# Kernel optimization log

Measured on AMD Instinct MI355X. Metric: run time of the kernel, lower is better.

## Reference

```python
import jax, jax.numpy as jnp
import numpy as np

B, S, D, V = 64, 128, 64, 50000

def _prelu(x, a):
    return jnp.where(x >= 0, x, a * x)

def setup_inputs() -> dict:
    key = jax.random.key(0)
    ks = jax.random.split(key, 24)
    stdv = 1.0 / np.sqrt(D)
    u = lambda k, shape: jax.random.uniform(k, shape, jnp.float32, -stdv, stdv)
    emb = u(ks[0], (V, D)).at[0].set(0.0)  # padding_idx=0
    inp = {
        'items': jax.random.randint(ks[1], (B, S), 0, V),
        'A': jax.random.randint(ks[2], (B, S, S), 0, 2),
        'edgeorder': jax.random.randint(ks[3], (B, S, S), 0, S),
        'last_nodes': jax.random.randint(ks[4], (B,), 0, S),
        'mask': jnp.ones((B, S), dtype=bool),
        'emb': emb,
        'W_self': u(ks[5], (D, D)), 'W_neigh': u(ks[6], (D, D)),
        'prelu1': jnp.full((D,), 0.25, jnp.float32),
        'Wq': u(ks[7], (D, D)), 'bq': jnp.zeros((D,), jnp.float32),
        'Wk': u(ks[8], (D, D)), 'Wv': u(ks[9], (D, D)), 'we': u(ks[10], (D,)),
        'prelu2': jnp.full((D,), 0.25, jnp.float32),
        'Wu': u(ks[11], (D, D)), 'bu': jnp.zeros((D,), jnp.float32),
        'Wvr': u(ks[12], (D, D)), 'wer': u(ks[13], (D,)),
        'prelu3': jnp.full((D,), 0.25, jnp.float32),
        'W_sr': u(ks[14], (2 * D, D)),
    }
    return inp

def reference(items, A, edgeorder, last_nodes, mask, emb, W_self, W_neigh, prelu1,
              Wq, bq, Wk, Wv, we, prelu2, Wu, bu, Wvr, wer, prelu3, W_sr):
    x = emb[items]  # [B,S,D]
    # ---- EOPA: masked neighbor broadcast + edgeorder gather + max-pool ----
    adjT = (jnp.swapaxes(A, 1, 2) == 1)  # [B,S(target),S(neighbor)]
    neigh = jnp.where((adjT & mask[:, None, :])[..., None], x[:, None, :, :], 0.0)  # [B,S,S,D]
    eo_t = jnp.swapaxes(edgeorder, 1, 2)  # [B,S,S]
    # gathered[b,i,j,:] = neigh[b, edgeorder[b,j,i], j, :]
    neigh = jnp.take_along_axis(neigh, eo_t[..., None], axis=1)
    neigh = neigh.max(axis=2)  # [B,S,D]
    h = _prelu(x @ W_self + neigh @ W_neigh, prelu1)
    # ---- SGAT: sigmoid-gated attention over adjacency ----
    q = h @ Wq + bq
    k = h @ Wk
    v = h @ Wv
    e = k[:, :, None, :] + q[:, None, :, :]             # e[b,i,j,d]
    e = jnp.where((A == 1)[..., None], e, 0.0)
    e = jax.nn.sigmoid(e) @ we                           # [B,S,S]
    a = jax.nn.softmax(e, axis=1)                        # softmax over source i
    h2 = _prelu(jnp.einsum('bij,bid->bjd', a, v), prelu2)
    # ---- AttnReadout ----
    xu = h2 @ Wu + bu                                    # [B,S,D]
    xlast = h2[jnp.arange(h2.shape[0]), last_nodes]      # [B,D]
    xv = xlast @ Wvr
    eatt = jax.nn.sigmoid(xu + xv[:, None, :]) @ wer     # [B,S]
    alpha = jax.nn.softmax(eatt, axis=1)
    out = _prelu((h2 * alpha[..., None]).sum(axis=1), prelu3)  # [B,D]
    # ---- session representation ----
    sr = jnp.concatenate([out, xlast], axis=-1) @ W_sr   # [B,D]
    return sr
```

## Files before the change

### kernel.cpp

```cpp
#include <hip/hip_runtime.h>

#define BB 64
#define SS 128
#define DD 64
#define SSQ (SS*SS)
#define BSD (BB*SS*DD)

__device__ __forceinline__ float fast_sigmoid(float x) {
  return __builtin_amdgcn_rcpf(1.0f + __expf(-x));
}

__global__ __launch_bounds__(256) void kA(
    const int* __restrict__ items, const int* __restrict__ Aadj,
    const int* __restrict__ eo, const float* __restrict__ emb,
    const float* __restrict__ Wself, const float* __restrict__ Wneigh,
    const float* __restrict__ prelu1,
    const float* __restrict__ Wq, const float* __restrict__ bq,
    const float* __restrict__ Wk, const float* __restrict__ Wv,
    float* __restrict__ q_ws, float* __restrict__ k_ws, float* __restrict__ v_ws)
{
  __shared__ alignas(16) float xs[SS*DD];
  __shared__ alignas(16) float Wb[2][DD*DD];
  __shared__ alignas(16) float nms[16*DD];
  __shared__ alignas(16) float hs[16*DD];
  __shared__ unsigned short condw[SS];
  const int b  = blockIdx.x >> 3;
  const int i0 = (blockIdx.x & 7) * 16;
  const int tid = threadIdx.x;
  const int wv = tid >> 6, lane = tid & 63;

  {
    const float4* emb4 = (const float4*)emb;
    float4* xs4 = (float4*)xs;
    for (int f = tid; f < SS*16; f += 256) {
      int j = f >> 4, qd = f & 15;
      xs4[f] = emb4[items[b*SS + j]*16 + qd];
    }
    const float4* W4 = (const float4*)Wself;
    float4* Wb4 = (float4*)Wb[0];
    for (int f = tid; f < 1024; f += 256) Wb4[f] = W4[f];
  }
  {
    int eov[8];
#pragma unroll
    for (int k = 0; k < 8; k++) {
      int p = tid + k*256;
      eov[k] = eo[b*SSQ + (p >> 4)*SS + i0 + (p & 15)];
    }
#pragma unroll
    for (int k = 0; k < 8; k++) {
      int p = tid + k*256;
      bool c = (Aadj[b*SSQ + (p >> 4)*SS + eov[k]] == 1);
      unsigned long long bm = __ballot(c);
      if ((lane & 15) == 0)
        condw[p >> 4] = (unsigned short)(bm >> lane);
    }
  }
  __syncthreads();

  {
    const float4* W4 = (const float4*)Wneigh;
    float4* Wb4 = (float4*)Wb[1];
    for (int f = tid; f < 1024; f += 256) Wb4[f] = W4[f];
  }
  {
    float m[4];
#pragma unroll
    for (int t = 0; t < 4; t++) m[t] = -__builtin_inff();
    for (int j = 0; j < SS; j++) {
      unsigned int cw = (unsigned int)condw[j] >> (wv*4);
      float xv = xs[j*DD + lane];
#pragma unroll
      for (int t = 0; t < 4; t++) {
        float val = ((cw >> t) & 1u) ? xv : 0.0f;
        m[t] = fmaxf(m[t], val);
      }
    }
#pragma unroll
    for (int t = 0; t < 4; t++) nms[(wv*4 + t)*DD + lane] = m[t];
  }
  float acc[4];
#pragma unroll
  for (int t = 0; t < 4; t++) acc[t] = 0.0f;
  for (int kk = 0; kk < DD; kk++) {
    float w = Wb[0][kk*DD + lane];
#pragma unroll
    for (int t = 0; t < 4; t++)
      acc[t] = fmaf(xs[(i0 + wv*4 + t)*DD + kk], w, acc[t]);
  }
  __syncthreads();

  {
    const float4* W4 = (const float4*)Wq;
    float4* Wb4 = (float4*)Wb[0];
    for (int f = tid; f < 1024; f += 256) Wb4[f] = W4[f];
  }
  for (int kk = 0; kk < DD; kk++) {
    float w = Wb[1][kk*DD + lane];
#pragma unroll
    for (int t = 0; t < 4; t++)
      acc[t] = fmaf(nms[(wv*4 + t)*DD + kk], w, acc[t]);
  }
  {
    float p1 = prelu1[lane];
#pragma unroll
    for (int t = 0; t < 4; t++) {
      float h = acc[t];
      hs[(wv*4 + t)*DD + lane] = (h >= 0.0f) ? h : p1*h;
    }
  }
  __syncthreads();

  const int r0g = b*SS + i0;
  {
    const float4* W4 = (const float4*)Wk;
    float4* Wb4 = (float4*)Wb[1];
    for (int f = tid; f < 1024; f += 256) Wb4[f] = W4[f];
  }
  {
    float bqv = bq[lane];
#pragma unroll
    for (int t = 0; t < 4; t++) acc[t] = bqv;
    for (int kk = 0; kk < DD; kk++) {
      float w = Wb[0][kk*DD + lane];
#pragma unroll
      for (int t = 0; t < 4; t++)
        acc[t] = fmaf(hs[(wv*4 + t)*DD + kk], w, acc[t]);
    }
#pragma unroll
    for (int t = 0; t < 4; t++) q_ws[(r0g + wv*4 + t)*DD + lane] = acc[t];
  }
  __syncthreads();

  {
    const float4* W4 = (const float4*)Wv;
    float4* Wb4 = (float4*)Wb[0];
    for (int f = tid; f < 1024; f += 256) Wb4[f] = W4[f];
  }
  {
#pragma unroll
    for (int t = 0; t < 4; t++) acc[t] = 0.0f;
    for (int kk = 0; kk < DD; kk++) {
      float w = Wb[1][kk*DD + lane];
#pragma unroll
      for (int t = 0; t < 4; t++)
        acc[t] = fmaf(hs[(wv*4 + t)*DD + kk], w, acc[t]);
    }
#pragma unroll
    for (int t = 0; t < 4; t++) k_ws[(r0g + wv*4 + t)*DD + lane] = acc[t];
  }
  __syncthreads();

  {
#pragma unroll
    for (int t = 0; t < 4; t++) acc[t] = 0.0f;
    for (int kk = 0; kk < DD; kk++) {
      float w = Wb[0][kk*DD + lane];
#pragma unroll
      for (int t = 0; t < 4; t++)
        acc[t] = fmaf(hs[(wv*4 + t)*DD + kk], w, acc[t]);
    }
#pragma unroll
    for (int t = 0; t < 4; t++) v_ws[(r0g + wv*4 + t)*DD + lane] = acc[t];
  }
}

__global__ __launch_bounds__(256) void kB(
    const int* __restrict__ Aadj,
    const float* __restrict__ q_ws, const float* __restrict__ k_ws,
    const float* __restrict__ v_ws,
    const float* __restrict__ we, const float* __restrict__ prelu2,
    const float* __restrict__ Wu, const float* __restrict__ bu,
    float* __restrict__ h2_ws, float* __restrict__ xu_ws)
{
  __shared__ alignas(16) float ks[SS*65];
  __shared__ alignas(16) float qs[16*65];
  __shared__ alignas(16) float es[16*129];
  __shared__ float wes[DD];
  const int b  = blockIdx.x >> 3;
  const int j0 = (blockIdx.x & 7) * 16;
  const int tid = threadIdx.x;
  const int wv = tid >> 6, lane = tid & 63;

  {
    const float4* k4 = (const float4*)k_ws;
    for (int f = tid; f < 2048; f += 256) {
      int i = f >> 4, d4 = f & 15;
      float4 v = k4[(b*SS + i)*16 + d4];
      float* dst = &ks[i*65 + d4*4];
      dst[0] = v.x; dst[1] = v.y; dst[2] = v.z; dst[3] = v.w;
    }
    const float4* q4 = (const float4*)q_ws;
    for (int f = tid; f < 256; f += 256) {
      int jl = f >> 4, d4 = f & 15;
      float4 v = q4[(b*SS + j0 + jl)*16 + d4];
      float* dst = &qs[jl*65 + d4*4];
      dst[0] = v.x; dst[1] = v.y; dst[2] = v.z; dst[3] = v.w;
    }
  }
  if (tid < DD) wes[tid] = we[tid];
  float hw = we[lane];
  for (int off = 32; off >= 1; off >>= 1) hw += __shfl_xor(hw, off);
  const float half_sum = 0.5f * hw;
  __syncthreads();

#pragma unroll
  for (int k = 0; k < 8; k++) {
    int p = tid + k*256;
    int jl = p & 15, i = p >> 4;
    float e2;
    if (Aadj[b*SSQ + i*SS + j0 + jl] == 1) {
      float s = 0.0f;
      for (int d2 = 0; d2 < DD; d2++) {
        float t = ks[i*65 + d2] + qs[jl*65 + d2];
        s = fmaf(wes[d2], fast_sigmoid(t), s);
      }
      e2 = s;
    } else {
      e2 = half_sum;
    }
    es[jl*129 + i] = e2;
  }
  __syncthreads();

  float* vs = ks;
  {
    const float4* v4 = (const float4*)v_ws;
    float4* vs4 = (float4*)vs;
    for (int f = tid; f < 2048; f += 256)
      vs4[f] = v4[b*SS*16 + f];
  }
#pragma unroll
  for (int t = 0; t < 4; t++) {
    int jl = wv*4 + t;
    float a0 = es[jl*129 + lane], a1 = es[jl*129 + 64 + lane];
    float mx = fmaxf(a0, a1);
    for (int off = 32; off >= 1; off >>= 1) mx = fmaxf(mx, __shfl_xor(mx, off));
    float p0 = __expf(a0 - mx), p1 = __expf(a1 - mx);
    float sm = p0 + p1;
    for (int off = 32; off >= 1; off >>= 1) sm += __shfl_xor(sm, off);
    float inv = 1.0f / sm;
    es[jl*129 + lane]      = p0 * inv;
    es[jl*129 + 64 + lane] = p1 * inv;
  }
  __syncthreads();

  float acc[4];
#pragma unroll
  for (int t = 0; t < 4; t++) acc[t] = 0.0f;
  for (int i = 0; i < SS; i++) {
    float vv = vs[i*DD + lane];
#pragma unroll
    for (int t = 0; t < 4; t++)
      acc[t] = fmaf(es[(wv*4 + t)*129 + i], vv, acc[t]);
  }
  float h2r[4];
  {
    float p2 = prelu2[lane];
#pragma unroll
    for (int t = 0; t < 4; t++) {
      float h2 = acc[t];
      h2r[t] = (h2 >= 0.0f) ? h2 : p2*h2;
      h2_ws[(b*SS + j0 + wv*4 + t)*DD + lane] = h2r[t];
    }
  }
  __syncthreads();

  float* hs2 = es;
  float* Wus = ks;
#pragma unroll
  for (int t = 0; t < 4; t++) hs2[(wv*4 + t)*DD + lane] = h2r[t];
  {
    const float4* W4 = (const float4*)Wu;
    float4* Wus4 = (float4*)Wus;
    for (int f = tid; f < 1024; f += 256) Wus4[f] = W4[f];
  }
  __syncthreads();
  {
    float buv = bu[lane];
    float acc2[4];
#pragma unroll
    for (int t = 0; t < 4; t++) acc2[t] = buv;
    for (int kk = 0; kk < DD; kk++) {
      float w = Wus[kk*DD + lane];
#pragma unroll
      for (int t = 0; t < 4; t++)
        acc2[t] = fmaf(hs2[(wv*4 + t)*DD + kk], w, acc2[t]);
    }
#pragma unroll
    for (int t = 0; t < 4; t++)
      xu_ws[(b*SS + j0 + wv*4 + t)*DD + lane] = acc2[t];
  }
}

__global__ __launch_bounds__(512) void k4_readout(
    const float* __restrict__ h2_ws, const float* __restrict__ xu_ws,
    const int* __restrict__ last_nodes,
    const float* __restrict__ Wvr, const float* __restrict__ wer,
    const float* __restrict__ prelu3, const float* __restrict__ Wsr,
    float* __restrict__ out)
{
  __shared__ float xlast[DD], xv[DD], eatt[SS], alpha[SS], outs[DD];
  __shared__ float pools[8*DD];
  const int b = blockIdx.x;
  const int tid = threadIdx.x;
  const int wv = tid >> 6, lane = tid & 63;

  const int ln = last_nodes[b];
  if (tid < DD) xlast[tid] = h2_ws[(b*SS + ln)*DD + tid];
  __syncthreads();
  if (tid < DD) {
    float s = 0.0f;
    for (int k2 = 0; k2 < DD; k2++)
      s = fmaf(xlast[k2], Wvr[k2*DD + tid], s);
    xv[tid] = s;
  }
  __syncthreads();
  {
    float werv = wer[lane];
    float xvl = xv[lane];
    for (int j = wv; j < SS; j += 8) {
      float xuv = xu_ws[(b*SS + j)*DD + lane];
      float term = fast_sigmoid(xuv + xvl) * werv;
      for (int off = 32; off >= 1; off >>= 1) term += __shfl_xor(term, off);
      if (lane == 0) eatt[j] = term;
    }
  }
  __syncthreads();
  if (wv == 0) {
    float a0 = eatt[lane], a1 = eatt[64 + lane];
    float mx = fmaxf(a0, a1);
    for (int off = 32; off >= 1; off >>= 1) mx = fmaxf(mx, __shfl_xor(mx, off));
    float p0 = __expf(a0 - mx), p1 = __expf(a1 - mx);
    float sm = p0 + p1;
    for (int off = 32; off >= 1; off >>= 1) sm += __shfl_xor(sm, off);
    float inv = 1.0f / sm;
    alpha[lane]      = p0 * inv;
    alpha[64 + lane] = p1 * inv;
  }
  __syncthreads();
  {
    float part = 0.0f;
    for (int j = wv; j < SS; j += 8)
      part = fmaf(alpha[j], h2_ws[(b*SS + j)*DD + lane], part);
    pools[wv*DD + lane] = part;
  }
  __syncthreads();
  if (wv == 0) {
    float s = 0.0f;
#pragma unroll
    for (int w = 0; w < 8; w++) s += pools[w*DD + lane];
    float p3 = prelu3[lane];
    outs[lane] = (s >= 0.0f) ? s : p3 * s;
  }
  __syncthreads();
  {
    float fs = 0.0f;
    for (int m2 = wv*16; m2 < wv*16 + 16; m2++) {
      float src = (m2 < DD) ? outs[m2] : xlast[m2 - DD];
      fs = fmaf(src, Wsr[m2*DD + lane], fs);
    }
    pools[wv*DD + lane] = fs;
  }
  __syncthreads();
  if (wv == 0) {
    float s = 0.0f;
#pragma unroll
    for (int w = 0; w < 8; w++) s += pools[w*DD + lane];
    out[b*DD + lane] = s;
  }
}

extern "C" void kernel_launch(void* const* d_in, const int* in_sizes, int n_in,
                              void* d_out, int out_size, void* d_ws, size_t ws_size,
                              hipStream_t stream)
{
  const int* items = (const int*)d_in[0];
  const int* Aadj  = (const int*)d_in[1];
  const int* eo    = (const int*)d_in[2];
  const int* lastn = (const int*)d_in[3];
  const float* emb    = (const float*)d_in[5];
  const float* Wself  = (const float*)d_in[6];
  const float* Wneigh = (const float*)d_in[7];
  const float* p1     = (const float*)d_in[8];
  const float* Wq     = (const float*)d_in[9];
  const float* bq     = (const float*)d_in[10];
  const float* Wk     = (const float*)d_in[11];
  const float* Wv     = (const float*)d_in[12];
  const float* we     = (const float*)d_in[13];
  const float* p2     = (const float*)d_in[14];
  const float* Wu     = (const float*)d_in[15];
  const float* bu     = (const float*)d_in[16];
  const float* Wvr    = (const float*)d_in[17];
  const float* wer    = (const float*)d_in[18];
  const float* p3     = (const float*)d_in[19];
  const float* Wsr    = (const float*)d_in[20];

  float* ws    = (float*)d_ws;
  float* q_ws  = ws;
  float* k_ws  = ws + (size_t)BSD;
  float* v_ws  = ws + (size_t)2*BSD;
  float* h2_ws = ws + (size_t)3*BSD;
  float* xu_ws = ws + (size_t)4*BSD;

  kA<<<BB*8, 256, 0, stream>>>(items, Aadj, eo, emb, Wself, Wneigh, p1,
                               Wq, bq, Wk, Wv, q_ws, k_ws, v_ws);
  kB<<<BB*8, 256, 0, stream>>>(Aadj, q_ws, k_ws, v_ws, we, p2, Wu, bu,
                               h2_ws, xu_ws);
  k4_readout<<<BB, 512, 0, stream>>>(h2_ws, xu_ws, lastn, Wvr, wer, p3, Wsr,
                                     (float*)d_out);
}
```

Baseline: 183.8 us.

## Halve rows per block, use readlane matvecs, drop LDS weight staging

Kernels kA and kB now handle 8 rows per block instead of 16, doubling the grid to 1024 blocks and cutting LDS use so more blocks fit per CU. Weight matrices are read directly from global/L2 rather than staged in shared memory. Per-row activations stay in registers and are broadcast with readlane, which removes several __syncthreads and LDS round trips. kB also makes the sigmoid loop branch-free, and the readout spreads the Wvr matvec across all waves. The cost is that each block reloads the full 128-row key/value set and the embeddings, and the weights are refetched from global memory instead of LDS.

```diff
diff --git a/kernel.cpp b/kernel.cpp
--- a/kernel.cpp
+++ b/kernel.cpp
@@ -9,8 +9,11 @@
 __device__ __forceinline__ float fast_sigmoid(float x) {
   return __builtin_amdgcn_rcpf(1.0f + __expf(-x));
 }
-
-__global__ __launch_bounds__(256) void kA(
+__device__ __forceinline__ float rl(float v, int l) {
+  return __int_as_float(__builtin_amdgcn_readlane(__float_as_int(v), l));
+}
+
+__global__ __launch_bounds__(256, 4) void kA(
     const int* __restrict__ items, const int* __restrict__ Aadj,
     const int* __restrict__ eo, const float* __restrict__ emb,
     const float* __restrict__ Wself, const float* __restrict__ Wneigh,
@@ -20,12 +23,9 @@
     float* __restrict__ q_ws, float* __restrict__ k_ws, float* __restrict__ v_ws)
 {
   __shared__ alignas(16) float xs[SS*DD];
-  __shared__ alignas(16) float Wb[2][DD*DD];
-  __shared__ alignas(16) float nms[16*DD];
-  __shared__ alignas(16) float hs[16*DD];
-  __shared__ unsigned short condw[SS];
-  const int b  = blockIdx.x >> 3;
-  const int i0 = (blockIdx.x & 7) * 16;
+  __shared__ unsigned char condw[SS];
+  const int b  = blockIdx.x >> 4;
+  const int i0 = (blockIdx.x & 15) * 8;
   const int tid = threadIdx.x;
   const int wv = tid >> 6, lane = tid & 63;
 
@@ -36,136 +36,102 @@
       int j = f >> 4, qd = f & 15;
       xs4[f] = emb4[items[b*SS + j]*16 + qd];
     }
-    const float4* W4 = (const float4*)Wself;
-    float4* Wb4 = (float4*)Wb[0];
-    for (int f = tid; f < 1024; f += 256) Wb4[f] = W4[f];
-  }
-  {
-    int eov[8];
-#pragma unroll
-    for (int k = 0; k < 8; k++) {
-      int p = tid + k*256;
-      eov[k] = eo[b*SSQ + (p >> 4)*SS + i0 + (p & 15)];
-    }
-#pragma unroll
-    for (int k = 0; k < 8; k++) {
-      int p = tid + k*256;
-      bool c = (Aadj[b*SSQ + (p >> 4)*SS + eov[k]] == 1);
+  }
+  {
+    int eov[4];
+#pragma unroll
+    for (int kq = 0; kq < 4; kq++) {
+      int p = tid + kq*256;
+      eov[kq] = eo[b*SSQ + (p >> 3)*SS + i0 + (p & 7)];
+    }
+#pragma unroll
+    for (int kq = 0; kq < 4; kq++) {
+      int p = tid + kq*256;
+      bool c = (Aadj[b*SSQ + (p >> 3)*SS + eov[kq]] == 1);
       unsigned long long bm = __ballot(c);
-      if ((lane & 15) == 0)
-        condw[p >> 4] = (unsigned short)(bm >> lane);
-    }
-  }
-  __syncthreads();
-
-  {
-    const float4* W4 = (const float4*)Wneigh;
-    float4* Wb4 = (float4*)Wb[1];
-    for (int f = tid; f < 1024; f += 256) Wb4[f] = W4[f];
-  }
-  {
-    float m[4];
-#pragma unroll
-    for (int t = 0; t < 4; t++) m[t] = -__builtin_inff();
-    for (int j = 0; j < SS; j++) {
-      unsigned int cw = (unsigned int)condw[j] >> (wv*4);
-      float xv = xs[j*DD + lane];
-#pragma unroll
-      for (int t = 0; t < 4; t++) {
-        float val = ((cw >> t) & 1u) ? xv : 0.0f;
-        m[t] = fmaxf(m[t], val);
-      }
-    }
-#pragma unroll
-    for (int t = 0; t < 4; t++) nms[(wv*4 + t)*DD + lane] = m[t];
-  }
-  float acc[4];
-#pragma unroll
-  for (int t = 0; t < 4; t++) acc[t] = 0.0f;
+      if ((lane & 7) == 0)
+        condw[p >> 3] = (unsigned char)(bm >> lane);
+    }
+  }
+  __syncthreads();
+
+  float m[2];
+#pragma unroll
+  for (int t = 0; t < 2; t++) m[t] = -__builtin_inff();
+  for (int j = 0; j < SS; j++) {
+    unsigned int cw = (unsigned int)condw[j] >> (wv*2);
+    float xv = xs[j*DD + lane];
+#pragma unroll
+    for (int t = 0; t < 2; t++) {
+      float val = ((cw >> t) & 1u) ? xv : 0.0f;
+      m[t] = fmaxf(m[t], val);
+    }
+  }
+  float xr[2];
+#pragma unroll
+  for (int t = 0; t < 2; t++) xr[t] = xs[(i0 + wv*2 + t)*DD + lane];
+
+  float acc[2] = {0.0f, 0.0f};
+#pragma unroll 8
   for (int kk = 0; kk < DD; kk++) {
-    float w = Wb[0][kk*DD + lane];
-#pragma unroll
-    for (int t = 0; t < 4; t++)
-      acc[t] = fmaf(xs[(i0 + wv*4 + t)*DD + kk], w, acc[t]);
-  }
-  __syncthreads();
-
-  {
-    const float4* W4 = (const float4*)Wq;
-    float4* Wb4 = (float4*)Wb[0];
-    for (int f = tid; f < 1024; f += 256) Wb4[f] = W4[f];
-  }
+    float w = Wself[kk*DD + lane];
+#pragma unroll
+    for (int t = 0; t < 2; t++) acc[t] = fmaf(rl(xr[t], kk), w, acc[t]);
+  }
+#pragma unroll 8
   for (int kk = 0; kk < DD; kk++) {
-    float w = Wb[1][kk*DD + lane];
-#pragma unroll
-    for (int t = 0; t < 4; t++)
-      acc[t] = fmaf(nms[(wv*4 + t)*DD + kk], w, acc[t]);
-  }
+    float w = Wneigh[kk*DD + lane];
+#pragma unroll
+    for (int t = 0; t < 2; t++) acc[t] = fmaf(rl(m[t], kk), w, acc[t]);
+  }
+  float hr[2];
   {
     float p1 = prelu1[lane];
 #pragma unroll
-    for (int t = 0; t < 4; t++) {
+    for (int t = 0; t < 2; t++) {
       float h = acc[t];
-      hs[(wv*4 + t)*DD + lane] = (h >= 0.0f) ? h : p1*h;
-    }
-  }
-  __syncthreads();
-
-  const int r0g = b*SS + i0;
-  {
-    const float4* W4 = (const float4*)Wk;
-    float4* Wb4 = (float4*)Wb[1];
-    for (int f = tid; f < 1024; f += 256) Wb4[f] = W4[f];
-  }
+      hr[t] = (h >= 0.0f) ? h : p1*h;
+    }
+  }
+
+  const int r0g = b*SS + i0 + wv*2;
   {
     float bqv = bq[lane];
-#pragma unroll
-    for (int t = 0; t < 4; t++) acc[t] = bqv;
+    float a2[2] = {bqv, bqv};
+#pragma unroll 8
     for (int kk = 0; kk < DD; kk++) {
-      float w = Wb[0][kk*DD + lane];
-#pragma unroll
-      for (int t = 0; t < 4; t++)
-        acc[t] = fmaf(hs[(wv*4 + t)*DD + kk], w, acc[t]);
-    }
-#pragma unroll
-    for (int t = 0; t < 4; t++) q_ws[(r0g + wv*4 + t)*DD + lane] = acc[t];
-  }
-  __syncthreads();
-
-  {
-    const float4* W4 = (const float4*)Wv;
-    float4* Wb4 = (float4*)Wb[0];
-    for (int f = tid; f < 1024; f += 256) Wb4[f] = W4[f];
-  }
-  {
-#pragma unroll
-    for (int t = 0; t < 4; t++) acc[t] = 0.0f;
+      float w = Wq[kk*DD + lane];
+#pragma unroll
+      for (int t = 0; t < 2; t++) a2[t] = fmaf(rl(hr[t], kk), w, a2[t]);
+    }
+#pragma unroll
+    for (int t = 0; t < 2; t++) q_ws[(r0g + t)*DD + lane] = a2[t];
+  }
+  {
+    float a2[2] = {0.0f, 0.0f};
+#pragma unroll 8
     for (int kk = 0; kk < DD; kk++) {
-      float w = Wb[1][kk*DD + lane];
-#pragma unroll
-      for (int t = 0; t < 4; t++)
-        acc[t] = fmaf(hs[(wv*4 + t)*DD + kk], w, acc[t]);
-    }
-#pragma unroll
-    for (int t = 0; t < 4; t++) k_ws[(r0g + wv*4 + t)*DD + lane] = acc[t];
-  }
-  __syncthreads();
-
-  {
-#pragma unroll
-    for (int t = 0; t < 4; t++) acc[t] = 0.0f;
+      float w = Wk[kk*DD + lane];
+#pragma unroll
+      for (int t = 0; t < 2; t++) a2[t] = fmaf(rl(hr[t], kk), w, a2[t]);
+    }
+#pragma unroll
+    for (int t = 0; t < 2; t++) k_ws[(r0g + t)*DD + lane] = a2[t];
+  }
+  {
+    float a2[2] = {0.0f, 0.0f};
+#pragma unroll 8
     for (int kk = 0; kk < DD; kk++) {
-      float w = Wb[0][kk*DD + lane];
-#pragma unroll
-      for (int t = 0; t < 4; t++)
-        acc[t] = fmaf(hs[(wv*4 + t)*DD + kk], w, acc[t]);
-    }
-#pragma unroll
-    for (int t = 0; t < 4; t++) v_ws[(r0g + wv*4 + t)*DD + lane] = acc[t];
-  }
-}
-
-__global__ __launch_bounds__(256) void kB(
+      float w = Wv[kk*DD + lane];
+#pragma unroll
+      for (int t = 0; t < 2; t++) a2[t] = fmaf(rl(hr[t], kk), w, a2[t]);
+    }
+#pragma unroll
+    for (int t = 0; t < 2; t++) v_ws[(r0g + t)*DD + lane] = a2[t];
+  }
+}
+
+__global__ __launch_bounds__(256, 4) void kB(
     const int* __restrict__ Aadj,
     const float* __restrict__ q_ws, const float* __restrict__ k_ws,
     const float* __restrict__ v_ws,
@@ -174,11 +140,11 @@
     float* __restrict__ h2_ws, float* __restrict__ xu_ws)
 {
   __shared__ alignas(16) float ks[SS*65];
-  __shared__ alignas(16) float qs[16*65];
-  __shared__ alignas(16) float es[16*129];
+  __shared__ alignas(16) float qs[8*65];
+  __shared__ alignas(16) float es[8*129];
   __shared__ float wes[DD];
-  const int b  = blockIdx.x >> 3;
-  const int j0 = (blockIdx.x & 7) * 16;
+  const int b  = blockIdx.x >> 4;
+  const int j0 = (blockIdx.x & 15) * 8;
   const int tid = threadIdx.x;
   const int wv = tid >> 6, lane = tid & 63;
 
@@ -191,35 +157,30 @@
       dst[0] = v.x; dst[1] = v.y; dst[2] = v.z; dst[3] = v.w;
     }
     const float4* q4 = (const float4*)q_ws;
-    for (int f = tid; f < 256; f += 256) {
-      int jl = f >> 4, d4 = f & 15;
+    if (tid < 128) {
+      int jl = tid >> 4, d4 = tid & 15;
       float4 v = q4[(b*SS + j0 + jl)*16 + d4];
       float* dst = &qs[jl*65 + d4*4];
       dst[0] = v.x; dst[1] = v.y; dst[2] = v.z; dst[3] = v.w;
     }
-  }
-  if (tid < DD) wes[tid] = we[tid];
+    if (tid < DD) wes[tid] = we[tid];
+  }
   float hw = we[lane];
   for (int off = 32; off >= 1; off >>= 1) hw += __shfl_xor(hw, off);
   const float half_sum = 0.5f * hw;
   __syncthreads();
 
 #pragma unroll
-  for (int k = 0; k < 8; k++) {
-    int p = tid + k*256;
-    int jl = p & 15, i = p >> 4;
-    float e2;
-    if (Aadj[b*SSQ + i*SS + j0 + jl] == 1) {
-      float s = 0.0f;
-      for (int d2 = 0; d2 < DD; d2++) {
-        float t = ks[i*65 + d2] + qs[jl*65 + d2];
-        s = fmaf(wes[d2], fast_sigmoid(t), s);
-      }
-      e2 = s;
-    } else {
-      e2 = half_sum;
-    }
-    es[jl*129 + i] = e2;
+  for (int kq = 0; kq < 4; kq++) {
+    int p = tid + kq*256;
+    int jl = p & 7, i = p >> 3;
+    bool isE = (Aadj[b*SSQ + i*SS + j0 + jl] == 1);
+    float s = 0.0f;
+    for (int d2 = 0; d2 < DD; d2++) {
+      float t = ks[i*65 + d2] + qs[jl*65 + d2];
+      s = fmaf(wes[d2], fast_sigmoid(t), s);
+    }
+    es[jl*129 + i] = isE ? s : half_sum;
   }
   __syncthreads();
 
@@ -230,9 +191,10 @@
     for (int f = tid; f < 2048; f += 256)
       vs4[f] = v4[b*SS*16 + f];
   }
-#pragma unroll
-  for (int t = 0; t < 4; t++) {
-    int jl = wv*4 + t;
+  float a0n[2], a1n[2];
+#pragma unroll
+  for (int t = 0; t < 2; t++) {
+    int jl = wv*2 + t;
     float a0 = es[jl*129 + lane], a1 = es[jl*129 + 64 + lane];
     float mx = fmaxf(a0, a1);
     for (int off = 32; off >= 1; off >>= 1) mx = fmaxf(mx, __shfl_xor(mx, off));
@@ -240,56 +202,44 @@
     float sm = p0 + p1;
     for (int off = 32; off >= 1; off >>= 1) sm += __shfl_xor(sm, off);
     float inv = 1.0f / sm;
-    es[jl*129 + lane]      = p0 * inv;
-    es[jl*129 + 64 + lane] = p1 * inv;
-  }
-  __syncthreads();
-
-  float acc[4];
-#pragma unroll
-  for (int t = 0; t < 4; t++) acc[t] = 0.0f;
-  for (int i = 0; i < SS; i++) {
+    a0n[t] = p0 * inv;
+    a1n[t] = p1 * inv;
+  }
+  __syncthreads();
+
+  float acc[2] = {0.0f, 0.0f};
+  for (int i = 0; i < 64; i++) {
     float vv = vs[i*DD + lane];
 #pragma unroll
-    for (int t = 0; t < 4; t++)
-      acc[t] = fmaf(es[(wv*4 + t)*129 + i], vv, acc[t]);
-  }
-  float h2r[4];
+    for (int t = 0; t < 2; t++) acc[t] = fmaf(rl(a0n[t], i), vv, acc[t]);
+  }
+  for (int i = 0; i < 64; i++) {
+    float vv = vs[(64 + i)*DD + lane];
+#pragma unroll
+    for (int t = 0; t < 2; t++) acc[t] = fmaf(rl(a1n[t], i), vv, acc[t]);
+  }
+  float h2r[2];
   {
     float p2 = prelu2[lane];
 #pragma unroll
-    for (int t = 0; t < 4; t++) {
+    for (int t = 0; t < 2; t++) {
       float h2 = acc[t];
       h2r[t] = (h2 >= 0.0f) ? h2 : p2*h2;
-      h2_ws[(b*SS + j0 + wv*4 + t)*DD + lane] = h2r[t];
-    }
-  }
-  __syncthreads();
-
-  float* hs2 = es;
-  float* Wus = ks;
-#pragma unroll
-  for (int t = 0; t < 4; t++) hs2[(wv*4 + t)*DD + lane] = h2r[t];
-  {
-    const float4* W4 = (const float4*)Wu;
-    float4* Wus4 = (float4*)Wus;
-    for (int f = tid; f < 1024; f += 256) Wus4[f] = W4[f];
-  }
-  __syncthreads();
+      h2_ws[(b*SS + j0 + wv*2 + t)*DD + lane] = h2r[t];
+    }
+  }
   {
     float buv = bu[lane];
-    float acc2[4];
-#pragma unroll
-    for (int t = 0; t < 4; t++) acc2[t] = buv;
+    float a2[2] = {buv, buv};
+#pragma unroll 8
     for (int kk = 0; kk < DD; kk++) {
-      float w = Wus[kk*DD + lane];
-#pragma unroll
-      for (int t = 0; t < 4; t++)
-        acc2[t] = fmaf(hs2[(wv*4 + t)*DD + kk], w, acc2[t]);
-    }
-#pragma unroll
-    for (int t = 0; t < 4; t++)
-      xu_ws[(b*SS + j0 + wv*4 + t)*DD + lane] = acc2[t];
+      float w = Wu[kk*DD + lane];
+#pragma unroll
+      for (int t = 0; t < 2; t++) a2[t] = fmaf(rl(h2r[t], kk), w, a2[t]);
+    }
+#pragma unroll
+    for (int t = 0; t < 2; t++)
+      xu_ws[(b*SS + j0 + wv*2 + t)*DD + lane] = a2[t];
   }
 }
 
@@ -309,11 +259,21 @@
   const int ln = last_nodes[b];
   if (tid < DD) xlast[tid] = h2_ws[(b*SS + ln)*DD + tid];
   __syncthreads();
-  if (tid < DD) {
-    float s = 0.0f;
-    for (int k2 = 0; k2 < DD; k2++)
-      s = fmaf(xlast[k2], Wvr[k2*DD + tid], s);
-    xv[tid] = s;
+  {
+    float s = 0.0f;
+#pragma unroll
+    for (int r = 0; r < 8; r++) {
+      int k2 = wv*8 + r;
+      s = fmaf(xlast[k2], Wvr[k2*DD + lane], s);
+    }
+    pools[wv*DD + lane] = s;
+  }
+  __syncthreads();
+  if (wv == 0) {
+    float s = 0.0f;
+#pragma unroll
+    for (int w = 0; w < 8; w++) s += pools[w*DD + lane];
+    xv[lane] = s;
   }
   __syncthreads();
   {
@@ -356,7 +316,9 @@
   __syncthreads();
   {
     float fs = 0.0f;
-    for (int m2 = wv*16; m2 < wv*16 + 16; m2++) {
+#pragma unroll
+    for (int r = 0; r < 16; r++) {
+      int m2 = wv*16 + r;
       float src = (m2 < DD) ? outs[m2] : xlast[m2 - DD];
       fs = fmaf(src, Wsr[m2*DD + lane], fs);
     }
@@ -403,10 +365,10 @@
   float* h2_ws = ws + (size_t)3*BSD;
   float* xu_ws = ws + (size_t)4*BSD;
 
-  kA<<<BB*8, 256, 0, stream>>>(items, Aadj, eo, emb, Wself, Wneigh, p1,
-                               Wq, bq, Wk, Wv, q_ws, k_ws, v_ws);
-  kB<<<BB*8, 256, 0, stream>>>(Aadj, q_ws, k_ws, v_ws, we, p2, Wu, bu,
-                               h2_ws, xu_ws);
+  kA<<<BB*16, 256, 0, stream>>>(items, Aadj, eo, emb, Wself, Wneigh, p1,
+                                Wq, bq, Wk, Wv, q_ws, k_ws, v_ws);
+  kB<<<BB*16, 256, 0, stream>>>(Aadj, q_ws, k_ws, v_ws, we, p2, Wu, bu,
+                                h2_ws, xu_ws);
   k4_readout<<<BB, 512, 0, stream>>>(h2_ws, xu_ws, lastn, Wvr, wer, p3, Wsr,
                                      (float*)d_out);
 }
```

Result: no change. 185.6 us (+1.0%).
